# Optimization experiments

Measured on AMD Instinct MI355X. Metric: run time of the kernel, lower is better.

The kernel has to match this reference:

```python
import jax, jax.numpy as jnp
import numpy as np

N_NODES = 100000
N_EDGES = 1600000
D = 64        # input_dim_nodes == input_dim_edges == output_dim
H = 128       # hidden_dim
LN_EPS = 1e-5


def setup_inputs() -> dict:
    key = jax.random.key(0)
    ks = jax.random.split(key, 9)
    efeat = jax.random.normal(ks[0], (N_EDGES, D), dtype=jnp.float32)
    nfeat = jax.random.normal(ks[1], (N_NODES, D), dtype=jnp.float32)
    dst_idx = jax.random.randint(ks[2], (N_EDGES,), 0, N_NODES, dtype=jnp.int32)
    s1 = 1.0 / np.sqrt(2 * D)
    s2 = 1.0 / np.sqrt(H)
    W1 = jax.random.normal(ks[3], (2 * D, H), dtype=jnp.float32) * s1
    b1 = jnp.zeros((H,), jnp.float32)
    W2 = jax.random.normal(ks[4], (H, D), dtype=jnp.float32) * s2
    b2 = jnp.zeros((D,), jnp.float32)
    gamma = jnp.ones((D,), jnp.float32)
    beta = jnp.zeros((D,), jnp.float32)
    return {"efeat": efeat, "nfeat": nfeat, "dst_idx": dst_idx,
            "W1": W1, "b1": b1, "W2": W2, "b2": b2,
            "gamma": gamma, "beta": beta}


def _layer_norm(x, gamma, beta):
    mu = jnp.mean(x, axis=-1, keepdims=True)
    var = jnp.mean(jnp.square(x - mu), axis=-1, keepdims=True)
    return (x - mu) * jax.lax.rsqrt(var + LN_EPS) * gamma + beta


def reference(efeat, nfeat, dst_idx, W1, b1, W2, b2, gamma, beta):
    # scatter-sum edge features into destination nodes: [E,D] -> [N,D]
    agg = jax.ops.segment_sum(efeat, dst_idx, num_segments=N_NODES)
    # concat(aggregated_edge_feat, node_feat) -> [N, 2D]
    cat_feat = jnp.concatenate([agg, nfeat], axis=-1)
    # MLP: Linear -> SiLU -> Linear -> LayerNorm
    h = jax.nn.silu(cat_feat @ W1 + b1)
    h = h @ W2 + b2
    nfeat_new = _layer_norm(h, gamma, beta) + nfeat
    return (efeat, nfeat_new)
```

## Files before the change

kernel.cpp:

```cpp
#include <hip/hip_runtime.h>
#include <hip/hip_bf16.h>
#include <math.h>

#define N_NODES 100000
#define N_EDGES 1600000
#define D 64
#define H 128
#define LN_EPS 1e-5f

#define NCHUNK ((N_NODES + 1023) / 1024)

__global__ void zero_cnt(int* __restrict__ cnt) {
    int i = blockIdx.x * blockDim.x + threadIdx.x;
    if (i < N_NODES) cnt[i] = 0;
}

__global__ void hist(const int* __restrict__ dst, int* __restrict__ cnt) {
    const int stride = gridDim.x * blockDim.x;
    for (int e = blockIdx.x * blockDim.x + threadIdx.x; e < N_EDGES; e += stride)
        atomicAdd(&cnt[dst[e]], 1);
}

__global__ void scan1(const int* __restrict__ cnt,
                      int* __restrict__ starts,
                      int* __restrict__ chunkSum) {
    __shared__ int ps[256];
    const int t = threadIdx.x;
    const int base = blockIdx.x * 1024 + t * 4;
    int v[4];
    #pragma unroll
    for (int r = 0; r < 4; ++r)
        v[r] = (base + r < N_NODES) ? cnt[base + r] : 0;
    int s = v[0] + v[1] + v[2] + v[3];
    ps[t] = s;
    __syncthreads();
    for (int off = 1; off < 256; off <<= 1) {
        int x = (t >= off) ? ps[t - off] : 0;
        __syncthreads();
        ps[t] += x;
        __syncthreads();
    }
    int run = (t > 0) ? ps[t - 1] : 0;
    #pragma unroll
    for (int r = 0; r < 4; ++r) {
        if (base + r < N_NODES) starts[base + r] = run;
        run += v[r];
    }
    if (t == 255) chunkSum[blockIdx.x] = ps[255];
}

__global__ void scan2(const int* __restrict__ chunkSum,
                      int* __restrict__ chunkOff) {
    __shared__ int ps[128];
    const int t = threadIdx.x;
    int own = (t < NCHUNK) ? chunkSum[t] : 0;
    ps[t] = own;
    __syncthreads();
    for (int off = 1; off < 128; off <<= 1) {
        int x = (t >= off) ? ps[t - off] : 0;
        __syncthreads();
        ps[t] += x;
        __syncthreads();
    }
    chunkOff[t] = ps[t] - own;
}

__global__ void scan3(int* __restrict__ starts,
                      const int* __restrict__ chunkOff,
                      int* __restrict__ cursor) {
    const int stride = gridDim.x * blockDim.x;
    for (int i = blockIdx.x * blockDim.x + threadIdx.x; i < N_NODES; i += stride) {
        int s = starts[i] + chunkOff[i >> 10];
        starts[i] = s;
        cursor[i] = s;
    }
}

__global__ void bin_edges(const int* __restrict__ dst,
                          int* __restrict__ cursor,
                          int* __restrict__ eidx) {
    const int stride = gridDim.x * blockDim.x;
    for (int e = blockIdx.x * blockDim.x + threadIdx.x; e < N_EDGES; e += stride) {
        int pos = atomicAdd(&cursor[dst[e]], 1);
        eidx[pos] = e;
    }
}

__device__ __forceinline__ float silu_f(float x) {
    return x / (1.f + __expf(-x));
}

__global__ __launch_bounds__(512, 4)
void fused_mlp(const float4* __restrict__ ef4, float4* __restrict__ out4,
               const float* __restrict__ nfeat,
               const int* __restrict__ starts, const int* __restrict__ cnt,
               const int* __restrict__ eidx,
               const float* __restrict__ W1, const float* __restrict__ b1,
               const float* __restrict__ W2, const float* __restrict__ b2,
               const float* __restrict__ gamma, const float* __restrict__ beta,
               float* __restrict__ out_n) {
    __shared__ float XT[128][132];

    const int tid  = threadIdx.x;
    const int lane = tid & 63;
    const int wave = tid >> 6;
    const int rg   = lane >> 4;
    const int q    = lane & 15;
    const int nbase = blockIdx.x * 128;

    const float gl = gamma[lane];
    const float bl = beta[lane];

    float nf[16];
    #pragma unroll 1
    for (int i = 0; i < 16; ++i) {
        const int col = wave * 16 + i;
        const int n = nbase + col;
        if (n < N_NODES) {
            const int st  = __builtin_amdgcn_readfirstlane(starts[n]);
            const int deg = __builtin_amdgcn_readfirstlane(cnt[n]);
            float4 acc = make_float4(0.f, 0.f, 0.f, 0.f);
            for (int base = 0; base < deg; base += 64) {
                const int m = min(deg - base, 64);
                int eid_l = (lane < m) ? eidx[st + base + lane] : 0;
                for (int c = 0; c < m; c += 4) {
                    const int row = c + rg;
                    const int id = __shfl(eid_l, row);
                    if (row < m) {
                        float4 v = ef4[id * 16 + q];
                        out4[id * 16 + q] = v;
                        acc.x += v.x; acc.y += v.y; acc.z += v.z; acc.w += v.w;
                    }
                }
            }
            acc.x += __shfl_xor(acc.x, 16); acc.y += __shfl_xor(acc.y, 16);
            acc.z += __shfl_xor(acc.z, 16); acc.w += __shfl_xor(acc.w, 16);
            acc.x += __shfl_xor(acc.x, 32); acc.y += __shfl_xor(acc.y, 32);
            acc.z += __shfl_xor(acc.z, 32); acc.w += __shfl_xor(acc.w, 32);
            if (lane < 16) {
                XT[q * 4 + 0][col] = acc.x;
                XT[q * 4 + 1][col] = acc.y;
                XT[q * 4 + 2][col] = acc.z;
                XT[q * 4 + 3][col] = acc.w;
            }
            const float nv = nfeat[(long long)n * D + lane];
            XT[64 + lane][col] = nv;
            nf[i] = nv;
        } else {
            if (lane < 16) {
                XT[q * 4 + 0][col] = 0.f; XT[q * 4 + 1][col] = 0.f;
                XT[q * 4 + 2][col] = 0.f; XT[q * 4 + 3][col] = 0.f;
            }
            XT[64 + lane][col] = 0.f;
            nf[i] = 0.f;
        }
    }
    __syncthreads();

    const int nt = tid & 15;
    const int j0 = (tid >> 4) * 4;

    float acc0[4][4], acc1[4][4];
    {
        const float4 b4 = *(const float4*)(b1 + j0);
        const float bj[4] = {b4.x, b4.y, b4.z, b4.w};
        #pragma unroll
        for (int i = 0; i < 4; ++i)
            #pragma unroll
            for (int j = 0; j < 4; ++j) { acc0[i][j] = bj[j]; acc1[i][j] = bj[j]; }
    }
    #pragma unroll 4
    for (int k = 0; k < 2 * D; ++k) {
        const float4 w4 = *(const float4*)(W1 + k * H + j0);
        const float4 xa = *(const float4*)(&XT[k][nt * 4]);
        const float4 xb = *(const float4*)(&XT[k][64 + nt * 4]);
        const float wv[4] = {w4.x, w4.y, w4.z, w4.w};
        const float av[4] = {xa.x, xa.y, xa.z, xa.w};
        const float bv[4] = {xb.x, xb.y, xb.z, xb.w};
        #pragma unroll
        for (int i = 0; i < 4; ++i)
            #pragma unroll
            for (int j = 0; j < 4; ++j) {
                acc0[i][j] = fmaf(av[i], wv[j], acc0[i][j]);
                acc1[i][j] = fmaf(bv[i], wv[j], acc1[i][j]);
            }
    }
    __syncthreads();

    #pragma unroll
    for (int j = 0; j < 4; ++j) {
        *(float4*)(&XT[j0 + j][nt * 4]) =
            make_float4(silu_f(acc0[0][j]), silu_f(acc0[1][j]),
                        silu_f(acc0[2][j]), silu_f(acc0[3][j]));
        *(float4*)(&XT[j0 + j][64 + nt * 4]) =
            make_float4(silu_f(acc1[0][j]), silu_f(acc1[1][j]),
                        silu_f(acc1[2][j]), silu_f(acc1[3][j]));
    }
    __syncthreads();

    const int d0 = (tid >> 4) * 2;
    float o0[4][2], o1[4][2];
    {
        const float2 b2v = *(const float2*)(b2 + d0);
        #pragma unroll
        for (int i = 0; i < 4; ++i) {
            o0[i][0] = b2v.x; o0[i][1] = b2v.y;
            o1[i][0] = b2v.x; o1[i][1] = b2v.y;
        }
    }
    #pragma unroll 4
    for (int h = 0; h < H; ++h) {
        const float2 w2v = *(const float2*)(W2 + h * D + d0);
        const float4 sa = *(const float4*)(&XT[h][nt * 4]);
        const float4 sb = *(const float4*)(&XT[h][64 + nt * 4]);
        const float sav[4] = {sa.x, sa.y, sa.z, sa.w};
        const float sbv[4] = {sb.x, sb.y, sb.z, sb.w};
        #pragma unroll
        for (int i = 0; i < 4; ++i) {
            o0[i][0] = fmaf(sav[i], w2v.x, o0[i][0]);
            o0[i][1] = fmaf(sav[i], w2v.y, o0[i][1]);
            o1[i][0] = fmaf(sbv[i], w2v.x, o1[i][0]);
            o1[i][1] = fmaf(sbv[i], w2v.y, o1[i][1]);
        }
    }
    __syncthreads();

    float* O = &XT[0][0];
    #pragma unroll
    for (int i = 0; i < 4; ++i) {
        *(float2*)(O + (nt * 4 + i) * 66 + d0)      = make_float2(o0[i][0], o0[i][1]);
        *(float2*)(O + (64 + nt * 4 + i) * 66 + d0) = make_float2(o1[i][0], o1[i][1]);
    }
    __syncthreads();

    #pragma unroll 1
    for (int i = 0; i < 16; ++i) {
        const int col = wave * 16 + i;
        const int gn = nbase + col;
        float x = O[col * 66 + lane];
        float s = x, qq = x * x;
        #pragma unroll
        for (int off = 32; off > 0; off >>= 1) {
            s  += __shfl_xor(s,  off);
            qq += __shfl_xor(qq, off);
        }
        const float mu  = s * (1.f / 64.f);
        const float var = qq * (1.f / 64.f) - mu * mu;
        const float rs  = rsqrtf(var + LN_EPS);
        if (gn < N_NODES)
            out_n[(long long)gn * D + lane] = (x - mu) * rs * gl + bl + nf[i];
    }
}

extern "C" void kernel_launch(void* const* d_in, const int* in_sizes, int n_in,
                              void* d_out, int out_size, void* d_ws, size_t ws_size,
                              hipStream_t stream) {
    const float* efeat = (const float*)d_in[0];
    const float* nfeat = (const float*)d_in[1];
    const int*   dst   = (const int*)  d_in[2];
    const float* W1    = (const float*)d_in[3];
    const float* b1    = (const float*)d_in[4];
    const float* W2    = (const float*)d_in[5];
    const float* b2    = (const float*)d_in[6];
    const float* gamma = (const float*)d_in[7];
    const float* beta  = (const float*)d_in[8];

    float* out_e = (float*)d_out;
    float* out_n = (float*)d_out + (long long)N_EDGES * D;

    int* eidx   = (int*)d_ws;
    int* cnt    = eidx + N_EDGES;
    int* starts = cnt + N_NODES;
    int* cursor = starts + N_NODES;
    int* chunkSum = cursor + N_NODES;
    int* chunkOff = chunkSum + 128;

    zero_cnt <<<(N_NODES + 255) / 256, 256, 0, stream>>>(cnt);
    hist     <<<1024, 256, 0, stream>>>(dst, cnt);
    scan1    <<<NCHUNK, 256, 0, stream>>>(cnt, starts, chunkSum);
    scan2    <<<1, 128, 0, stream>>>(chunkSum, chunkOff);
    scan3    <<<512, 256, 0, stream>>>(starts, chunkOff, cursor);
    bin_edges<<<2048, 256, 0, stream>>>(dst, cursor, eidx);
    fused_mlp<<<(N_NODES + 127) / 128, 512, 0, stream>>>(
        (const float4*)efeat, (float4*)out_e, nfeat,
        starts, cnt, eidx, W1, b1, W2, b2, gamma, beta, out_n);
}
```

Before: 1.100 ms.

## Prefetch edge indices per wave and switch MLP smem to swizzled row-major tiles

Degree is now taken from adjacent CSR starts, with a sentinel written at the end, so the cnt read goes away. Each wave loads its 16 starts and first-64 edge indices up front to expose memory parallelism before the gather loop. Shared memory switches from a transposed layout to node-major rows with an XOR swizzle, and the GEMM tiles are reshaped to 4x8 and 4x4 outputs per thread. nfeat is re-read from global memory in the LayerNorm epilogue instead of being kept in registers. Grid sizes for hist and bin_edges are doubled. Fully unrolled loops holding eidv[16] raise register pressure under launch_bounds(512,4).

```diff
diff --git a/kernel.cpp b/kernel.cpp
--- a/kernel.cpp
+++ b/kernel.cpp
@@ -7,8 +7,8 @@
 #define D 64
 #define H 128
 #define LN_EPS 1e-5f
-
 #define NCHUNK ((N_NODES + 1023) / 1024)
+
 
 __global__ void zero_cnt(int* __restrict__ cnt) {
     int i = blockIdx.x * blockDim.x + threadIdx.x;
@@ -68,8 +68,10 @@
 __global__ void scan3(int* __restrict__ starts,
                       const int* __restrict__ chunkOff,
                       int* __restrict__ cursor) {
+    const int gid = blockIdx.x * blockDim.x + threadIdx.x;
+    if (gid == 0) starts[N_NODES] = N_EDGES;
     const int stride = gridDim.x * blockDim.x;
-    for (int i = blockIdx.x * blockDim.x + threadIdx.x; i < N_NODES; i += stride) {
+    for (int i = gid; i < N_NODES; i += stride) {
         int s = starts[i] + chunkOff[i >> 10];
         starts[i] = s;
         cursor[i] = s;
@@ -93,13 +95,12 @@
 __global__ __launch_bounds__(512, 4)
 void fused_mlp(const float4* __restrict__ ef4, float4* __restrict__ out4,
                const float* __restrict__ nfeat,
-               const int* __restrict__ starts, const int* __restrict__ cnt,
-               const int* __restrict__ eidx,
+               const int* __restrict__ starts, const int* __restrict__ eidx,
                const float* __restrict__ W1, const float* __restrict__ b1,
                const float* __restrict__ W2, const float* __restrict__ b2,
                const float* __restrict__ gamma, const float* __restrict__ beta,
                float* __restrict__ out_n) {
-    __shared__ float XT[128][132];
+    __shared__ float B[128 * 132];
 
     const int tid  = threadIdx.x;
     const int lane = tid & 63;
@@ -108,136 +109,166 @@
     const int q    = lane & 15;
     const int nbase = blockIdx.x * 128;
 
+    int sv = 0;
+    {
+        const int idx = nbase + wave * 16 + lane;
+        if (lane <= 16 && idx <= N_NODES) sv = starts[idx];
+    }
+    int eidv[16];
+    #pragma unroll
+    for (int i = 0; i < 16; ++i) {
+        const int st = __shfl(sv, i);
+        const int dg = __shfl(sv, i + 1) - st;
+        eidv[i] = (lane < dg) ? eidx[st + lane] : 0;
+        const int col = wave * 16 + i;
+        const int n = nbase + col;
+        const float nv = (n < N_NODES) ? nfeat[n * D + lane] : 0.f;
+        const int g = ((16 + (lane >> 2)) ^ ((col >> 2) & 31)) & 31;
+        B[col * 132 + g * 4 + (lane & 3)] = nv;
+    }
+
+    #pragma unroll
+    for (int i = 0; i < 16; ++i) {
+        const int col = wave * 16 + i;
+        const int st = __shfl(sv, i);
+        const int dg = __shfl(sv, i + 1) - st;
+        float4 a = make_float4(0.f, 0.f, 0.f, 0.f);
+        const int m = dg < 64 ? dg : 64;
+        for (int c = 0; c < m; c += 4) {
+            const int r = c + rg;
+            const int eid = __shfl(eidv[i], r);
+            if (r < m) {
+                const float4 v = ef4[eid * 16 + q];
+                out4[eid * 16 + q] = v;
+                a.x += v.x; a.y += v.y; a.z += v.z; a.w += v.w;
+            }
+        }
+        for (int bb = 64; bb < dg; bb += 64) {
+            const int rem = dg - bb;
+            int e2 = (lane < rem) ? eidx[st + bb + lane] : 0;
+            const int m2 = rem < 64 ? rem : 64;
+            for (int c = 0; c < m2; c += 4) {
+                const int r = c + rg;
+                const int eid = __shfl(e2, r);
+                if (r < m2) {
+                    const float4 v = ef4[eid * 16 + q];
+                    out4[eid * 16 + q] = v;
+                    a.x += v.x; a.y += v.y; a.z += v.z; a.w += v.w;
+                }
+            }
+        }
+        a.x += __shfl_xor(a.x, 16); a.y += __shfl_xor(a.y, 16);
+        a.z += __shfl_xor(a.z, 16); a.w += __shfl_xor(a.w, 16);
+        a.x += __shfl_xor(a.x, 32); a.y += __shfl_xor(a.y, 32);
+        a.z += __shfl_xor(a.z, 32); a.w += __shfl_xor(a.w, 32);
+        if (lane < 16) {
+            const int g = (q ^ ((col >> 2) & 31)) & 31;
+            *(float4*)&B[col * 132 + g * 4] = a;
+        }
+    }
+    __syncthreads();
+
+    const int nt = tid & 31;
+    const int jg = tid >> 5;
+    const int j0 = jg * 8;
+
+    float acc[4][8];
+    {
+        const float4 bA = *(const float4*)(b1 + j0);
+        const float4 bB = *(const float4*)(b1 + j0 + 4);
+        #pragma unroll
+        for (int i = 0; i < 4; ++i) {
+            acc[i][0] = bA.x; acc[i][1] = bA.y; acc[i][2] = bA.z; acc[i][3] = bA.w;
+            acc[i][4] = bB.x; acc[i][5] = bB.y; acc[i][6] = bB.z; acc[i][7] = bB.w;
+        }
+    }
+    #pragma unroll 2
+    for (int kq = 0; kq < 32; ++kq) {
+        const int g = (kq ^ nt) & 31;
+        float xv[4][4];
+        #pragma unroll
+        for (int i = 0; i < 4; ++i) {
+            const float4 x4 = *(const float4*)&B[(nt * 4 + i) * 132 + g * 4];
+            xv[i][0] = x4.x; xv[i][1] = x4.y; xv[i][2] = x4.z; xv[i][3] = x4.w;
+        }
+        #pragma unroll
+        for (int kk = 0; kk < 4; ++kk) {
+            const int k = kq * 4 + kk;
+            const float4 wA = *(const float4*)(W1 + k * H + j0);
+            const float4 wB = *(const float4*)(W1 + k * H + j0 + 4);
+            const float wv[8] = {wA.x, wA.y, wA.z, wA.w, wB.x, wB.y, wB.z, wB.w};
+            #pragma unroll
+            for (int i = 0; i < 4; ++i)
+                #pragma unroll
+                for (int j = 0; j < 8; ++j)
+                    acc[i][j] = fmaf(xv[i][kk], wv[j], acc[i][j]);
+        }
+    }
+    __syncthreads();
+
+    #pragma unroll
+    for (int i = 0; i < 4; ++i) {
+        const int n = nt * 4 + i;
+        const int g0 = ((jg * 2)     ^ nt) & 31;
+        const int g1 = ((jg * 2 + 1) ^ nt) & 31;
+        *(float4*)&B[n * 132 + g0 * 4] =
+            make_float4(silu_f(acc[i][0]), silu_f(acc[i][1]),
+                        silu_f(acc[i][2]), silu_f(acc[i][3]));
+        *(float4*)&B[n * 132 + g1 * 4] =
+            make_float4(silu_f(acc[i][4]), silu_f(acc[i][5]),
+                        silu_f(acc[i][6]), silu_f(acc[i][7]));
+    }
+    __syncthreads();
+
+    const int dg = tid >> 5;
+    const int d0 = dg * 4;
+    float o[4][4];
+    {
+        const float4 b4 = *(const float4*)(b2 + d0);
+        #pragma unroll
+        for (int i = 0; i < 4; ++i) {
+            o[i][0] = b4.x; o[i][1] = b4.y; o[i][2] = b4.z; o[i][3] = b4.w;
+        }
+    }
+    #pragma unroll 2
+    for (int hq = 0; hq < 32; ++hq) {
+        const int g = (hq ^ nt) & 31;
+        float sv4[4][4];
+        #pragma unroll
+        for (int i = 0; i < 4; ++i) {
+            const float4 s4 = *(const float4*)&B[(nt * 4 + i) * 132 + g * 4];
+            sv4[i][0] = s4.x; sv4[i][1] = s4.y; sv4[i][2] = s4.z; sv4[i][3] = s4.w;
+        }
+        #pragma unroll
+        for (int hh = 0; hh < 4; ++hh) {
+            const int h = hq * 4 + hh;
+            const float4 w = *(const float4*)(W2 + h * D + d0);
+            const float wv[4] = {w.x, w.y, w.z, w.w};
+            #pragma unroll
+            for (int i = 0; i < 4; ++i)
+                #pragma unroll
+                for (int dd = 0; dd < 4; ++dd)
+                    o[i][dd] = fmaf(sv4[i][hh], wv[dd], o[i][dd]);
+        }
+    }
+    __syncthreads();
+
+    #pragma unroll
+    for (int i = 0; i < 4; ++i) {
+        const int n = nt * 4 + i;
+        const int g = (dg ^ nt) & 15;
+        *(float4*)&B[n * 68 + g * 4] = make_float4(o[i][0], o[i][1], o[i][2], o[i][3]);
+    }
+    __syncthreads();
+
     const float gl = gamma[lane];
     const float bl = beta[lane];
-
-    float nf[16];
-    #pragma unroll 1
-    for (int i = 0; i < 16; ++i) {
-        const int col = wave * 16 + i;
-        const int n = nbase + col;
-        if (n < N_NODES) {
-            const int st  = __builtin_amdgcn_readfirstlane(starts[n]);
-            const int deg = __builtin_amdgcn_readfirstlane(cnt[n]);
-            float4 acc = make_float4(0.f, 0.f, 0.f, 0.f);
-            for (int base = 0; base < deg; base += 64) {
-                const int m = min(deg - base, 64);
-                int eid_l = (lane < m) ? eidx[st + base + lane] : 0;
-                for (int c = 0; c < m; c += 4) {
-                    const int row = c + rg;
-                    const int id = __shfl(eid_l, row);
-                    if (row < m) {
-                        float4 v = ef4[id * 16 + q];
-                        out4[id * 16 + q] = v;
-                        acc.x += v.x; acc.y += v.y; acc.z += v.z; acc.w += v.w;
-                    }
-                }
-            }
-            acc.x += __shfl_xor(acc.x, 16); acc.y += __shfl_xor(acc.y, 16);
-            acc.z += __shfl_xor(acc.z, 16); acc.w += __shfl_xor(acc.w, 16);
-            acc.x += __shfl_xor(acc.x, 32); acc.y += __shfl_xor(acc.y, 32);
-            acc.z += __shfl_xor(acc.z, 32); acc.w += __shfl_xor(acc.w, 32);
-            if (lane < 16) {
-                XT[q * 4 + 0][col] = acc.x;
-                XT[q * 4 + 1][col] = acc.y;
-                XT[q * 4 + 2][col] = acc.z;
-                XT[q * 4 + 3][col] = acc.w;
-            }
-            const float nv = nfeat[(long long)n * D + lane];
-            XT[64 + lane][col] = nv;
-            nf[i] = nv;
-        } else {
-            if (lane < 16) {
-                XT[q * 4 + 0][col] = 0.f; XT[q * 4 + 1][col] = 0.f;
-                XT[q * 4 + 2][col] = 0.f; XT[q * 4 + 3][col] = 0.f;
-            }
-            XT[64 + lane][col] = 0.f;
-            nf[i] = 0.f;
-        }
-    }
-    __syncthreads();
-
-    const int nt = tid & 15;
-    const int j0 = (tid >> 4) * 4;
-
-    float acc0[4][4], acc1[4][4];
-    {
-        const float4 b4 = *(const float4*)(b1 + j0);
-        const float bj[4] = {b4.x, b4.y, b4.z, b4.w};
-        #pragma unroll
-        for (int i = 0; i < 4; ++i)
-            #pragma unroll
-            for (int j = 0; j < 4; ++j) { acc0[i][j] = bj[j]; acc1[i][j] = bj[j]; }
-    }
-    #pragma unroll 4
-    for (int k = 0; k < 2 * D; ++k) {
-        const float4 w4 = *(const float4*)(W1 + k * H + j0);
-        const float4 xa = *(const float4*)(&XT[k][nt * 4]);
-        const float4 xb = *(const float4*)(&XT[k][64 + nt * 4]);
-        const float wv[4] = {w4.x, w4.y, w4.z, w4.w};
-        const float av[4] = {xa.x, xa.y, xa.z, xa.w};
-        const float bv[4] = {xb.x, xb.y, xb.z, xb.w};
-        #pragma unroll
-        for (int i = 0; i < 4; ++i)
-            #pragma unroll
-            for (int j = 0; j < 4; ++j) {
-                acc0[i][j] = fmaf(av[i], wv[j], acc0[i][j]);
-                acc1[i][j] = fmaf(bv[i], wv[j], acc1[i][j]);
-            }
-    }
-    __syncthreads();
-
-    #pragma unroll
-    for (int j = 0; j < 4; ++j) {
-        *(float4*)(&XT[j0 + j][nt * 4]) =
-            make_float4(silu_f(acc0[0][j]), silu_f(acc0[1][j]),
-                        silu_f(acc0[2][j]), silu_f(acc0[3][j]));
-        *(float4*)(&XT[j0 + j][64 + nt * 4]) =
-            make_float4(silu_f(acc1[0][j]), silu_f(acc1[1][j]),
-                        silu_f(acc1[2][j]), silu_f(acc1[3][j]));
-    }
-    __syncthreads();
-
-    const int d0 = (tid >> 4) * 2;
-    float o0[4][2], o1[4][2];
-    {
-        const float2 b2v = *(const float2*)(b2 + d0);
-        #pragma unroll
-        for (int i = 0; i < 4; ++i) {
-            o0[i][0] = b2v.x; o0[i][1] = b2v.y;
-            o1[i][0] = b2v.x; o1[i][1] = b2v.y;
-        }
-    }
-    #pragma unroll 4
-    for (int h = 0; h < H; ++h) {
-        const float2 w2v = *(const float2*)(W2 + h * D + d0);
-        const float4 sa = *(const float4*)(&XT[h][nt * 4]);
-        const float4 sb = *(const float4*)(&XT[h][64 + nt * 4]);
-        const float sav[4] = {sa.x, sa.y, sa.z, sa.w};
-        const float sbv[4] = {sb.x, sb.y, sb.z, sb.w};
-        #pragma unroll
-        for (int i = 0; i < 4; ++i) {
-            o0[i][0] = fmaf(sav[i], w2v.x, o0[i][0]);
-            o0[i][1] = fmaf(sav[i], w2v.y, o0[i][1]);
-            o1[i][0] = fmaf(sbv[i], w2v.x, o1[i][0]);
-            o1[i][1] = fmaf(sbv[i], w2v.y, o1[i][1]);
-        }
-    }
-    __syncthreads();
-
-    float* O = &XT[0][0];
-    #pragma unroll
-    for (int i = 0; i < 4; ++i) {
-        *(float2*)(O + (nt * 4 + i) * 66 + d0)      = make_float2(o0[i][0], o0[i][1]);
-        *(float2*)(O + (64 + nt * 4 + i) * 66 + d0) = make_float2(o1[i][0], o1[i][1]);
-    }
-    __syncthreads();
-
-    #pragma unroll 1
+    #pragma unroll
     for (int i = 0; i < 16; ++i) {
         const int col = wave * 16 + i;
         const int gn = nbase + col;
-        float x = O[col * 66 + lane];
+        const int g = ((lane >> 2) ^ ((col >> 2) & 15)) & 15;
+        float x = B[col * 68 + g * 4 + (lane & 3)];
         float s = x, qq = x * x;
         #pragma unroll
         for (int off = 32; off > 0; off >>= 1) {
@@ -247,8 +278,10 @@
         const float mu  = s * (1.f / 64.f);
         const float var = qq * (1.f / 64.f) - mu * mu;
         const float rs  = rsqrtf(var + LN_EPS);
-        if (gn < N_NODES)
-            out_n[(long long)gn * D + lane] = (x - mu) * rs * gl + bl + nf[i];
+        if (gn < N_NODES) {
+            const float nv = nfeat[(long long)gn * D + lane];
+            out_n[(long long)gn * D + lane] = (x - mu) * rs * gl + bl + nv;
+        }
     }
 }
 
@@ -268,20 +301,20 @@
     float* out_e = (float*)d_out;
     float* out_n = (float*)d_out + (long long)N_EDGES * D;
 
-    int* eidx   = (int*)d_ws;
-    int* cnt    = eidx + N_EDGES;
-    int* starts = cnt + N_NODES;
-    int* cursor = starts + N_NODES;
+    int* eidx     = (int*)d_ws;
+    int* cnt      = eidx + N_EDGES;
+    int* starts   = cnt + N_NODES;
+    int* cursor   = starts + (N_NODES + 1);
     int* chunkSum = cursor + N_NODES;
     int* chunkOff = chunkSum + 128;
 
     zero_cnt <<<(N_NODES + 255) / 256, 256, 0, stream>>>(cnt);
-    hist     <<<1024, 256, 0, stream>>>(dst, cnt);
+    hist     <<<2048, 256, 0, stream>>>(dst, cnt);
     scan1    <<<NCHUNK, 256, 0, stream>>>(cnt, starts, chunkSum);
     scan2    <<<1, 128, 0, stream>>>(chunkSum, chunkOff);
     scan3    <<<512, 256, 0, stream>>>(starts, chunkOff, cursor);
-    bin_edges<<<2048, 256, 0, stream>>>(dst, cursor, eidx);
+    bin_edges<<<4096, 256, 0, stream>>>(dst, cursor, eidx);
     fused_mlp<<<(N_NODES + 127) / 128, 512, 0, stream>>>(
         (const float4*)efeat, (float4*)out_e, nfeat,
-        starts, cnt, eidx, W1, b1, W2, b2, gamma, beta, out_n);
-}
+        starts, eidx, W1, b1, W2, b2, gamma, beta, out_n);
+}
```

After: 1.082 ms. No clear change (-1.7%).
